# Kernel tuning notes

Hardware: AMD Instinct MI355X
Metric: run time of the kernel (lower is better)

Reference implementation:

```python
import jax, jax.numpy as jnp
import numpy as np

H = 150  # hidden size
STEPS = 10


def setup_inputs() -> dict:
    key = jax.random.key(0)
    ks = jax.random.split(key, 5)
    inputx = jax.random.normal(ks[0], (16, 1, H), dtype=jnp.float32)
    W_ih = jax.random.normal(ks[1], (4 * H, H), dtype=jnp.float32) * (1.0 / np.sqrt(H))
    W_hh = jax.random.normal(ks[2], (4 * H, H), dtype=jnp.float32) * (1.0 / np.sqrt(H))
    b_ih = jax.random.normal(ks[3], (4 * H,), dtype=jnp.float32) * (1.0 / np.sqrt(H))
    b_hh = jax.random.normal(ks[4], (4 * H,), dtype=jnp.float32) * (1.0 / np.sqrt(H))
    return {"inputx": inputx, "W_ih": W_ih, "W_hh": W_hh, "b_ih": b_ih, "b_hh": b_hh, "x": 13}


def _lstm_forward(inputx, W_ih, W_hh, b_ih, b_hh, x):
    # xs: the 10 steps inputx[x-10], ..., inputx[x-1], each [1, H]
    xs = inputx[x - STEPS:x]
    h0 = jnp.zeros((1, H), dtype=inputx.dtype)
    c0 = jnp.zeros((1, H), dtype=inputx.dtype)

    def step(carry, xt):
        h, c = carry
        # PyTorch LSTMCell: gates in order (i, f, g, o)
        gates = xt @ W_ih.T + b_ih + h @ W_hh.T + b_hh  # [1, 4H]
        i_g, f_g, g_g, o_g = jnp.split(gates, 4, axis=-1)
        c_new = jax.nn.sigmoid(f_g) * c + jax.nn.sigmoid(i_g) * jnp.tanh(g_g)
        h_new = jax.nn.sigmoid(o_g) * jnp.tanh(c_new)
        return (h_new, c_new), None

    (h_t, _), _ = jax.lax.scan(step, (h0, c0), xs)
    return h_t  # [1, H]


def reference(inputx, W_ih, W_hh, b_ih, b_hh, x):
    return _lstm_forward(inputx, W_ih, W_hh, b_ih, b_hh, x)
```

## Files before the change

### kernel.cpp

```cpp
#include <hip/hip_runtime.h>
#include <hip/hip_fp16.h>
#include <math.h>

#define H 150
#define G 600
#define STEPS 10
#define NT 320
#define WPR 76
#define NPK (WPR * G)
#define NGXB 19
#define NPKB 109
#define NPREP (NGXB + NPKB)
#define GXW 16
#define MAGIC 0x13579BDFu

#define GXP_WORDS (G * GXW)
#define SLOT_OFF (GXP_WORDS + NPK)

typedef _Float16 half2v __attribute__((ext_vector_type(2)));

__device__ __forceinline__ float sigm(float x) {
    return __builtin_amdgcn_rcpf(1.0f + __expf(-x));
}
__device__ __forceinline__ float ftanh(float x) {
    return 1.0f - 2.0f * __builtin_amdgcn_rcpf(1.0f + __expf(2.0f * x));
}
__device__ __forceinline__ float dot2(float acc, unsigned w, unsigned h) {
#if __has_builtin(__builtin_amdgcn_fdot2)
    return __builtin_amdgcn_fdot2(__builtin_bit_cast(half2v, w),
                                  __builtin_bit_cast(half2v, h), acc, false);
#else
    half2v wv = __builtin_bit_cast(half2v, w);
    half2v hv = __builtin_bit_cast(half2v, h);
    return acc + (float)wv.x * (float)hv.x + (float)wv.y * (float)hv.y;
#endif
}
__device__ __forceinline__ unsigned short f2h(float x) {
    _Float16 h = (_Float16)x;
    return __builtin_bit_cast(unsigned short, h);
}

__device__ __forceinline__ void st_agent(unsigned* p, unsigned v) {
    __hip_atomic_store(p, v, __ATOMIC_RELAXED, __HIP_MEMORY_SCOPE_AGENT);
}
__device__ __forceinline__ void st_agent_f(float* p, float v) {
    __hip_atomic_store(p, v, __ATOMIC_RELAXED, __HIP_MEMORY_SCOPE_AGENT);
}
__device__ __forceinline__ unsigned ld_agent(const unsigned* p) {
    return __hip_atomic_load(p, __ATOMIC_RELAXED, __HIP_MEMORY_SCOPE_AGENT);
}

__device__ __forceinline__ int rowperm(int p) {
    int q = (p >= 300) ? p - 300 : p;
    int g = (q >> 1) + ((q & 1) ? 150 : 0);
    return g + ((p >= 300) ? 300 : 0);
}

__global__ __launch_bounds__(NT) void lstm_all(
    const float* __restrict__ inputx, const float* __restrict__ W_ih,
    const float* __restrict__ W_hh, const float* __restrict__ b_ih,
    const float* __restrict__ b_hh, const int* __restrict__ xp,
    float* __restrict__ gxp, unsigned* __restrict__ Wp,
    unsigned* __restrict__ slots, float* __restrict__ out)
{
    const int t   = threadIdx.x;
    const int blk = blockIdx.x;

    if (blk > 0) {
        const int p = blk - 1;
        if (p < NGXB) {
            int gid = p * NT + t;
            if (gid < STEPS * G) {
                int pos = gid / STEPS;
                int st  = gid - pos * STEPS;
                int g   = rowperm(pos);
                const float* xrow = inputx + (xp[0] - STEPS + st) * H;
                const float* wrow = W_ih + g * H;
                float a0 = 0.f, a1 = 0.f;
                #pragma unroll
                for (int k = 0; k < H; k += 2) {
                    float2 wv = *reinterpret_cast<const float2*>(wrow + k);
                    float2 xv = *reinterpret_cast<const float2*>(xrow + k);
                    a0 += wv.x * xv.x;
                    a1 += wv.y * xv.y;
                }
                st_agent_f(&gxp[pos * GXW + st], a0 + a1 + b_ih[g] + b_hh[g]);
            }
        } else {
            for (int i = (p - NGXB) * NT + t; i < NPK; i += NPKB * NT) {
                int jh  = i / 2400;
                int r   = i - jh * 2400;
                int pos = r >> 2;
                int j   = 4 * jh + (r & 3);
                unsigned v = 0;
                if (j < 75) {
                    const float* row = W_hh + rowperm(pos) * H + 2 * j;
                    v = ((unsigned)f2h(row[1]) << 16) | (unsigned)f2h(row[0]);
                }
                st_agent(&Wp[i], v);
            }
        }
        __syncthreads();
        if (t == 0) st_agent(&slots[p], MAGIC);
        return;
    }

    __shared__ __align__(16) unsigned short s_hh[2][160];

    const bool work = (t < 300);
    const bool odd  = (t & 1);
    const int pos0 = t;
    const int pos1 = 300 + t;

    unsigned w[2 * WPR];
    float gx0[STEPS], gx1[STEPS];

    auto load_all = [&]() {
        if (work) {
            const float* ra = gxp + pos0 * GXW;
            const float* rb = gxp + pos1 * GXW;
            float4 q0 = *reinterpret_cast<const float4*>(ra);
            float4 q1 = *reinterpret_cast<const float4*>(ra + 4);
            float2 q2 = *reinterpret_cast<const float2*>(ra + 8);
            float4 p0 = *reinterpret_cast<const float4*>(rb);
            float4 p1 = *reinterpret_cast<const float4*>(rb + 4);
            float2 p2 = *reinterpret_cast<const float2*>(rb + 8);
            gx0[0]=q0.x; gx0[1]=q0.y; gx0[2]=q0.z; gx0[3]=q0.w;
            gx0[4]=q1.x; gx0[5]=q1.y; gx0[6]=q1.z; gx0[7]=q1.w;
            gx0[8]=q2.x; gx0[9]=q2.y;
            gx1[0]=p0.x; gx1[1]=p0.y; gx1[2]=p0.z; gx1[3]=p0.w;
            gx1[4]=p1.x; gx1[5]=p1.y; gx1[6]=p1.z; gx1[7]=p1.w;
            gx1[8]=p2.x; gx1[9]=p2.y;
            const uint4* W4 = reinterpret_cast<const uint4*>(Wp);
            #pragma unroll
            for (int jh = 0; jh < 19; ++jh) {
                uint4 v = W4[jh * 600 + pos0];
                w[4 * jh] = v.x; w[4 * jh + 1] = v.y;
                w[4 * jh + 2] = v.z; w[4 * jh + 3] = v.w;
            }
            #pragma unroll
            for (int jh = 0; jh < 19; ++jh) {
                uint4 v = W4[jh * 600 + pos1];
                w[WPR + 4 * jh] = v.x; w[WPR + 4 * jh + 1] = v.y;
                w[WPR + 4 * jh + 2] = v.z; w[WPR + 4 * jh + 3] = v.w;
            }
        }
    };

    load_all();
    {
        unsigned short* sh = &s_hh[0][0];
        sh[t] = 0;
    }

    int ok = 1;
    if (t < NPREP) ok = (ld_agent(&slots[t]) == MAGIC) ? 1 : 0;
    if (__syncthreads_and(ok) == 0) {
        if (t < NPREP) {
            while (ld_agent(&slots[t]) != MAGIC) __builtin_amdgcn_s_sleep(2);
        }
        __syncthreads();
        __threadfence();
        load_all();
        __syncthreads();
    }

    float c = 0.f;
    const float sgn = odd ? -1.f : 2.f;

    auto act = [&](float d0, float d1, int st) {
        if (work) {
            float vA = sigm(d0);
            float e  = __expf(sgn * d1);
            float r  = __builtin_amdgcn_rcpf(1.f + e);
            float vB = odd ? r : fmaf(-2.f, r, 1.f);
            float sf = __shfl_xor(vA, 1);
            float cn = fmaf(sf, c, vA * vB);
            float ftc = ftanh(cn);
            float ftco = __shfl_xor(ftc, 1);
            if (!odd) c = cn;
            else {
                float h = vB * ftco;
                if (st == STEPS - 1) out[t >> 1] = h;
                else                 s_hh[st & 1][t >> 1] = f2h(h);
            }
        }
    };

    act(gx0[0], gx1[0], 0);
    __syncthreads();

    #pragma unroll 1
    for (int st = 1; st < STEPS; ++st) {
        float d0 = 0.f, d1 = 0.f;
        if (work) {
            const char* hb = reinterpret_cast<const char*>(s_hh[(st + 1) & 1]);
            float a0 = 0.f, a1 = 0.f, a2 = 0.f, a3 = 0.f;
            float b0 = 0.f, b1 = 0.f, b2 = 0.f, b3 = 0.f;
            #pragma unroll
            for (int cc = 0; cc < 19; ++cc) {
                float4 hv = *reinterpret_cast<const float4*>(hb + 16 * cc);
                unsigned h0 = __float_as_uint(hv.x);
                unsigned h1 = __float_as_uint(hv.y);
                unsigned h2 = __float_as_uint(hv.z);
                unsigned h3 = __float_as_uint(hv.w);
                a0 = dot2(a0, w[4 * cc],     h0);
                a1 = dot2(a1, w[4 * cc + 1], h1);
                a2 = dot2(a2, w[4 * cc + 2], h2);
                a3 = dot2(a3, w[4 * cc + 3], h3);
                b0 = dot2(b0, w[WPR + 4 * cc],     h0);
                b1 = dot2(b1, w[WPR + 4 * cc + 1], h1);
                b2 = dot2(b2, w[WPR + 4 * cc + 2], h2);
                b3 = dot2(b3, w[WPR + 4 * cc + 3], h3);
            }
            d0 = gx0[st] + (a0 + a1) + (a2 + a3);
            d1 = gx1[st] + (b0 + b1) + (b2 + b3);
        }
        act(d0, d1, st);
        if (st < STEPS - 1) __syncthreads();
    }
}

__global__ __launch_bounds__(640) void lstm_fused(
    const float* __restrict__ inputx, const float* __restrict__ W_ih,
    const float* __restrict__ W_hh, const float* __restrict__ b_ih,
    const float* __restrict__ b_hh, const int* __restrict__ xp,
    float* __restrict__ out)
{
    __shared__ float s_h[H];
    __shared__ float s_c[H];
    __shared__ float s_gate[G];
    __shared__ float s_x[STEPS * H];

    const int tid = threadIdx.x;
    if (tid < H) { s_h[tid] = 0.f; s_c[tid] = 0.f; }
    const int x0 = (xp[0] - STEPS) * H;
    for (int i = tid; i < STEPS * H; i += 640) s_x[i] = inputx[x0 + i];
    __syncthreads();

    for (int t = 0; t < STEPS; ++t) {
        if (tid < G) {
            const float* wi = W_ih + tid * H;
            const float* wh = W_hh + tid * H;
            float acc = b_ih[tid] + b_hh[tid];
            for (int k = 0; k < H; ++k)
                acc += wi[k] * s_x[t * H + k] + wh[k] * s_h[k];
            s_gate[tid] = acc;
        }
        __syncthreads();
        if (tid < H) {
            float ig = s_gate[tid], fg = s_gate[H + tid];
            float gg = s_gate[2 * H + tid], og = s_gate[3 * H + tid];
            float cn = sigm(fg) * s_c[tid] + sigm(ig) * ftanh(gg);
            s_c[tid] = cn;
            s_h[tid] = sigm(og) * ftanh(cn);
        }
        __syncthreads();
    }
    if (tid < H) out[tid] = s_h[tid];
}

extern "C" void kernel_launch(void* const* d_in, const int* in_sizes, int n_in,
                              void* d_out, int out_size, void* d_ws, size_t ws_size,
                              hipStream_t stream) {
    const float* inputx = (const float*)d_in[0];
    const float* W_ih   = (const float*)d_in[1];
    const float* W_hh   = (const float*)d_in[2];
    const float* b_ih   = (const float*)d_in[3];
    const float* b_hh   = (const float*)d_in[4];
    const int*   xp     = (const int*)d_in[5];
    float* out = (float*)d_out;

    const size_t need = (size_t)(SLOT_OFF + NPREP) * sizeof(unsigned);
    if (ws_size >= need) {
        float*    gxp   = (float*)d_ws;
        unsigned* Wp    = (unsigned*)d_ws + GXP_WORDS;
        unsigned* slots = (unsigned*)d_ws + SLOT_OFF;
        lstm_all<<<NPREP + 1, NT, 0, stream>>>(inputx, W_ih, W_hh, b_ih, b_hh,
                                               xp, gxp, Wp, slots, out);
    } else {
        lstm_fused<<<1, 640, 0, stream>>>(inputx, W_ih, W_hh, b_ih, b_hh, xp, out);
    }
}
```

Baseline: 17.33 us.

## Split the K dimension across thread pairs and combine gate partials by shuffle

The recurrent W_hh weights are repacked so each thread in a pair holds half of the hidden-size columns for all four gates of one unit, instead of full rows for two gate rows. Each thread now reads only half of h from LDS per step and computes four partial dot products. The partner's partials are added in through two lane shuffles. This halves LDS traffic per step, but each accumulator chain gets longer and the packing adds index math and shuffles.

```diff
diff --git a/kernel.cpp b/kernel.cpp
--- a/kernel.cpp
+++ b/kernel.cpp
@@ -6,8 +6,8 @@
 #define G 600
 #define STEPS 10
 #define NT 320
-#define WPR 76
-#define NPK (WPR * G)
+#define WPT 160
+#define NPK2 48000
 #define NGXB 19
 #define NPKB 109
 #define NPREP (NGXB + NPKB)
@@ -15,7 +15,7 @@
 #define MAGIC 0x13579BDFu
 
 #define GXP_WORDS (G * GXW)
-#define SLOT_OFF (GXP_WORDS + NPK)
+#define SLOT_OFF (GXP_WORDS + NPK2)
 
 typedef _Float16 half2v __attribute__((ext_vector_type(2)));
 
@@ -87,14 +87,19 @@
                 st_agent_f(&gxp[pos * GXW + st], a0 + a1 + b_ih[g] + b_hh[g]);
             }
         } else {
-            for (int i = (p - NGXB) * NT + t; i < NPK; i += NPKB * NT) {
-                int jh  = i / 2400;
-                int r   = i - jh * 2400;
-                int pos = r >> 2;
-                int j   = 4 * jh + (r & 3);
+            for (int i = (p - NGXB) * NT + t; i < NPK2; i += NPKB * NT) {
+                int j4   = i / 1200;
+                int r    = i - j4 * 1200;
+                int tpos = r >> 2;
+                int jl   = r & 3;
+                int m    = 4 * j4 + jl;
+                int gate = m / 40;
+                int kk   = m - gate * 40;
+                int u    = tpos >> 1;
+                int klo  = (tpos & 1) * 80 + 2 * kk;
                 unsigned v = 0;
-                if (j < 75) {
-                    const float* row = W_hh + rowperm(pos) * H + 2 * j;
+                if (klo < 150) {
+                    const float* row = W_hh + (gate * 150 + u) * H + klo;
                     v = ((unsigned)f2h(row[1]) << 16) | (unsigned)f2h(row[0]);
                 }
                 st_agent(&Wp[i], v);
@@ -109,16 +114,15 @@
 
     const bool work = (t < 300);
     const bool odd  = (t & 1);
-    const int pos0 = t;
-    const int pos1 = 300 + t;
-
-    unsigned w[2 * WPR];
+    const int khoff = odd ? 160 : 0;
+
+    unsigned w[WPT];
     float gx0[STEPS], gx1[STEPS];
 
     auto load_all = [&]() {
         if (work) {
-            const float* ra = gxp + pos0 * GXW;
-            const float* rb = gxp + pos1 * GXW;
+            const float* ra = gxp + t * GXW;
+            const float* rb = gxp + (300 + t) * GXW;
             float4 q0 = *reinterpret_cast<const float4*>(ra);
             float4 q1 = *reinterpret_cast<const float4*>(ra + 4);
             float2 q2 = *reinterpret_cast<const float2*>(ra + 8);
@@ -133,16 +137,10 @@
             gx1[8]=p2.x; gx1[9]=p2.y;
             const uint4* W4 = reinterpret_cast<const uint4*>(Wp);
             #pragma unroll
-            for (int jh = 0; jh < 19; ++jh) {
-                uint4 v = W4[jh * 600 + pos0];
-                w[4 * jh] = v.x; w[4 * jh + 1] = v.y;
-                w[4 * jh + 2] = v.z; w[4 * jh + 3] = v.w;
-            }
-            #pragma unroll
-            for (int jh = 0; jh < 19; ++jh) {
-                uint4 v = W4[jh * 600 + pos1];
-                w[WPR + 4 * jh] = v.x; w[WPR + 4 * jh + 1] = v.y;
-                w[WPR + 4 * jh + 2] = v.z; w[WPR + 4 * jh + 3] = v.w;
+            for (int j4 = 0; j4 < 40; ++j4) {
+                uint4 v = W4[j4 * 300 + t];
+                w[4 * j4]     = v.x; w[4 * j4 + 1] = v.y;
+                w[4 * j4 + 2] = v.z; w[4 * j4 + 3] = v.w;
             }
         }
     };
@@ -194,27 +192,39 @@
     for (int st = 1; st < STEPS; ++st) {
         float d0 = 0.f, d1 = 0.f;
         if (work) {
-            const char* hb = reinterpret_cast<const char*>(s_hh[(st + 1) & 1]);
-            float a0 = 0.f, a1 = 0.f, a2 = 0.f, a3 = 0.f;
-            float b0 = 0.f, b1 = 0.f, b2 = 0.f, b3 = 0.f;
+            const char* hb = reinterpret_cast<const char*>(s_hh[(st + 1) & 1])
+                           + khoff;
+            float P0 = 0.f, P1 = 0.f, P2 = 0.f, P3 = 0.f;
             #pragma unroll
-            for (int cc = 0; cc < 19; ++cc) {
+            for (int cc = 0; cc < 10; ++cc) {
                 float4 hv = *reinterpret_cast<const float4*>(hb + 16 * cc);
                 unsigned h0 = __float_as_uint(hv.x);
                 unsigned h1 = __float_as_uint(hv.y);
                 unsigned h2 = __float_as_uint(hv.z);
                 unsigned h3 = __float_as_uint(hv.w);
-                a0 = dot2(a0, w[4 * cc],     h0);
-                a1 = dot2(a1, w[4 * cc + 1], h1);
-                a2 = dot2(a2, w[4 * cc + 2], h2);
-                a3 = dot2(a3, w[4 * cc + 3], h3);
-                b0 = dot2(b0, w[WPR + 4 * cc],     h0);
-                b1 = dot2(b1, w[WPR + 4 * cc + 1], h1);
-                b2 = dot2(b2, w[WPR + 4 * cc + 2], h2);
-                b3 = dot2(b3, w[WPR + 4 * cc + 3], h3);
-            }
-            d0 = gx0[st] + (a0 + a1) + (a2 + a3);
-            d1 = gx1[st] + (b0 + b1) + (b2 + b3);
+                P0 = dot2(P0, w[      4*cc    ], h0);
+                P0 = dot2(P0, w[      4*cc + 1], h1);
+                P0 = dot2(P0, w[      4*cc + 2], h2);
+                P0 = dot2(P0, w[      4*cc + 3], h3);
+                P1 = dot2(P1, w[ 40 + 4*cc    ], h0);
+                P1 = dot2(P1, w[ 40 + 4*cc + 1], h1);
+                P1 = dot2(P1, w[ 40 + 4*cc + 2], h2);
+                P1 = dot2(P1, w[ 40 + 4*cc + 3], h3);
+                P2 = dot2(P2, w[ 80 + 4*cc    ], h0);
+                P2 = dot2(P2, w[ 80 + 4*cc + 1], h1);
+                P2 = dot2(P2, w[ 80 + 4*cc + 2], h2);
+                P2 = dot2(P2, w[ 80 + 4*cc + 3], h3);
+                P3 = dot2(P3, w[120 + 4*cc    ], h0);
+                P3 = dot2(P3, w[120 + 4*cc + 1], h1);
+                P3 = dot2(P3, w[120 + 4*cc + 2], h2);
+                P3 = dot2(P3, w[120 + 4*cc + 3], h3);
+            }
+            float s1 = odd ? P0 : P1;
+            float r1 = __shfl_xor(s1, 1);
+            float s2 = odd ? P2 : P3;
+            float r2 = __shfl_xor(s2, 1);
+            d0 = gx0[st] + (odd ? P1 : P0) + r1;
+            d1 = gx1[st] + (odd ? P3 : P2) + r2;
         }
         act(d0, d1, st);
         if (st < STEPS - 1) __syncthreads();
```

Result: no change. 17.07 us (-1.5%).

## Assign one gate row per thread with 640-thread blocks and 4-lane gate groups

Applied to the files above, without the earlier changes.

The recurrent block grows from 320 to 640 threads so each thread owns one gate row instead of two. Rows are permuted so the four gates (i,f,g,o) of a hidden unit sit in adjacent lanes and combine through xor shuffles. Prep blocks are rebalanced so each packing block handles at most one element per thread. This halves per-thread dot-product work and weight registers on the serial critical path, at the cost of more threads per barrier and extra shuffles.

```diff
diff --git a/kernel.cpp b/kernel.cpp
--- a/kernel.cpp
+++ b/kernel.cpp
@@ -5,11 +5,11 @@
 #define H 150
 #define G 600
 #define STEPS 10
-#define NT 320
+#define NT 640
 #define WPR 76
 #define NPK (WPR * G)
-#define NGXB 19
-#define NPKB 109
+#define NGXB 10
+#define NPKB 118
 #define NPREP (NGXB + NPKB)
 #define GXW 16
 #define MAGIC 0x13579BDFu
@@ -50,10 +50,8 @@
     return __hip_atomic_load(p, __ATOMIC_RELAXED, __HIP_MEMORY_SCOPE_AGENT);
 }
 
-__device__ __forceinline__ int rowperm(int p) {
-    int q = (p >= 300) ? p - 300 : p;
-    int g = (q >> 1) + ((q & 1) ? 150 : 0);
-    return g + ((p >= 300) ? 300 : 0);
+__device__ __forceinline__ int rowperm(int pos) {
+    return (pos & 3) * 150 + (pos >> 2);
 }
 
 __global__ __launch_bounds__(NT) void lstm_all(
@@ -87,11 +85,12 @@
                 st_agent_f(&gxp[pos * GXW + st], a0 + a1 + b_ih[g] + b_hh[g]);
             }
         } else {
-            for (int i = (p - NGXB) * NT + t; i < NPK; i += NPKB * NT) {
-                int jh  = i / 2400;
-                int r   = i - jh * 2400;
+            int i = (p - NGXB) * NT + t;
+            if (i < NPK) {
+                int j4  = i / 2400;
+                int r   = i - j4 * 2400;
                 int pos = r >> 2;
-                int j   = 4 * jh + (r & 3);
+                int j   = 4 * j4 + (r & 3);
                 unsigned v = 0;
                 if (j < 75) {
                     const float* row = W_hh + rowperm(pos) * H + 2 * j;
@@ -107,48 +106,34 @@
 
     __shared__ __align__(16) unsigned short s_hh[2][160];
 
-    const bool work = (t < 300);
-    const bool odd  = (t & 1);
-    const int pos0 = t;
-    const int pos1 = 300 + t;
-
-    unsigned w[2 * WPR];
-    float gx0[STEPS], gx1[STEPS];
+    const bool work = (t < G);
+    const int  q    = t & 3;
+    const int  u    = t >> 2;
+
+    unsigned w[WPR];
+    float gxr[STEPS];
 
     auto load_all = [&]() {
         if (work) {
-            const float* ra = gxp + pos0 * GXW;
-            const float* rb = gxp + pos1 * GXW;
+            const float* ra = gxp + t * GXW;
             float4 q0 = *reinterpret_cast<const float4*>(ra);
             float4 q1 = *reinterpret_cast<const float4*>(ra + 4);
             float2 q2 = *reinterpret_cast<const float2*>(ra + 8);
-            float4 p0 = *reinterpret_cast<const float4*>(rb);
-            float4 p1 = *reinterpret_cast<const float4*>(rb + 4);
-            float2 p2 = *reinterpret_cast<const float2*>(rb + 8);
-            gx0[0]=q0.x; gx0[1]=q0.y; gx0[2]=q0.z; gx0[3]=q0.w;
-            gx0[4]=q1.x; gx0[5]=q1.y; gx0[6]=q1.z; gx0[7]=q1.w;
-            gx0[8]=q2.x; gx0[9]=q2.y;
-            gx1[0]=p0.x; gx1[1]=p0.y; gx1[2]=p0.z; gx1[3]=p0.w;
-            gx1[4]=p1.x; gx1[5]=p1.y; gx1[6]=p1.z; gx1[7]=p1.w;
-            gx1[8]=p2.x; gx1[9]=p2.y;
+            gxr[0]=q0.x; gxr[1]=q0.y; gxr[2]=q0.z; gxr[3]=q0.w;
+            gxr[4]=q1.x; gxr[5]=q1.y; gxr[6]=q1.z; gxr[7]=q1.w;
+            gxr[8]=q2.x; gxr[9]=q2.y;
             const uint4* W4 = reinterpret_cast<const uint4*>(Wp);
             #pragma unroll
-            for (int jh = 0; jh < 19; ++jh) {
-                uint4 v = W4[jh * 600 + pos0];
-                w[4 * jh] = v.x; w[4 * jh + 1] = v.y;
-                w[4 * jh + 2] = v.z; w[4 * jh + 3] = v.w;
-            }
-            #pragma unroll
-            for (int jh = 0; jh < 19; ++jh) {
-                uint4 v = W4[jh * 600 + pos1];
-                w[WPR + 4 * jh] = v.x; w[WPR + 4 * jh + 1] = v.y;
-                w[WPR + 4 * jh + 2] = v.z; w[WPR + 4 * jh + 3] = v.w;
+            for (int j4 = 0; j4 < 19; ++j4) {
+                uint4 v = W4[j4 * 600 + t];
+                w[4 * j4]     = v.x; w[4 * j4 + 1] = v.y;
+                w[4 * j4 + 2] = v.z; w[4 * j4 + 3] = v.w;
             }
         }
     };
 
     load_all();
-    {
+    if (t < 320) {
         unsigned short* sh = &s_hh[0][0];
         sh[t] = 0;
     }
@@ -166,57 +151,47 @@
     }
 
     float c = 0.f;
-    const float sgn = odd ? -1.f : 2.f;
-
-    auto act = [&](float d0, float d1, int st) {
+    const float sgn = (q == 2) ? 2.f : -1.f;
+
+    auto act = [&](float d, int st) {
         if (work) {
-            float vA = sigm(d0);
-            float e  = __expf(sgn * d1);
-            float r  = __builtin_amdgcn_rcpf(1.f + e);
-            float vB = odd ? r : fmaf(-2.f, r, 1.f);
-            float sf = __shfl_xor(vA, 1);
-            float cn = fmaf(sf, c, vA * vB);
-            float ftc = ftanh(cn);
-            float ftco = __shfl_xor(ftc, 1);
-            if (!odd) c = cn;
-            else {
-                float h = vB * ftco;
-                if (st == STEPS - 1) out[t >> 1] = h;
-                else                 s_hh[st & 1][t >> 1] = f2h(h);
+            float e = __expf(sgn * d);
+            float r = __builtin_amdgcn_rcpf(1.f + e);
+            float v = (q == 2) ? fmaf(-2.f, r, 1.f) : r;
+            float x2 = __shfl_xor(v, 2);
+            float x1 = __shfl_xor(v, 1);
+            float cn = fmaf(x1, c, v * x2);
+            c = cn;
+            float th = ftanh(cn);
+            float th3 = __shfl_xor(th, 3);
+            if (q == 3) {
+                float h = v * th3;
+                if (st == STEPS - 1) out[u] = h;
+                else                 s_hh[st & 1][u] = f2h(h);
             }
         }
     };
 
-    act(gx0[0], gx1[0], 0);
+    act(gxr[0], 0);
     __syncthreads();
 
     #pragma unroll 1
     for (int st = 1; st < STEPS; ++st) {
-        float d0 = 0.f, d1 = 0.f;
+        float d = 0.f;
         if (work) {
             const char* hb = reinterpret_cast<const char*>(s_hh[(st + 1) & 1]);
             float a0 = 0.f, a1 = 0.f, a2 = 0.f, a3 = 0.f;
-            float b0 = 0.f, b1 = 0.f, b2 = 0.f, b3 = 0.f;
             #pragma unroll
             for (int cc = 0; cc < 19; ++cc) {
                 float4 hv = *reinterpret_cast<const float4*>(hb + 16 * cc);
-                unsigned h0 = __float_as_uint(hv.x);
-                unsigned h1 = __float_as_uint(hv.y);
-                unsigned h2 = __float_as_uint(hv.z);
-                unsigned h3 = __float_as_uint(hv.w);
-                a0 = dot2(a0, w[4 * cc],     h0);
-                a1 = dot2(a1, w[4 * cc + 1], h1);
-                a2 = dot2(a2, w[4 * cc + 2], h2);
-                a3 = dot2(a3, w[4 * cc + 3], h3);
-                b0 = dot2(b0, w[WPR + 4 * cc],     h0);
-                b1 = dot2(b1, w[WPR + 4 * cc + 1], h1);
-                b2 = dot2(b2, w[WPR + 4 * cc + 2], h2);
-                b3 = dot2(b3, w[WPR + 4 * cc + 3], h3);
-            }
-            d0 = gx0[st] + (a0 + a1) + (a2 + a3);
-            d1 = gx1[st] + (b0 + b1) + (b2 + b3);
-        }
-        act(d0, d1, st);
+                a0 = dot2(a0, w[4 * cc],     __float_as_uint(hv.x));
+                a1 = dot2(a1, w[4 * cc + 1], __float_as_uint(hv.y));
+                a2 = dot2(a2, w[4 * cc + 2], __float_as_uint(hv.z));
+                a3 = dot2(a3, w[4 * cc + 3], __float_as_uint(hv.w));
+            }
+            d = gxr[st] + (a0 + a1) + (a2 + a3);
+        }
+        act(d, st);
         if (st < STEPS - 1) __syncthreads();
     }
 }
```

After: 16.85 us. 2.8% less time.
